# Optimization experiments

Hardware: AMD Instinct MI355X
Metric: run time of the kernel (lower is better)

The kernel has to match this reference:

```python
import jax, jax.numpy as jnp
import numpy as np

N, E, B = 10000, 20000, 500
H, NODE_D, EDGE_D, L = 64, 11, 5, 3
BN_EPS = 1e-5
STEPS = 3  # Set2Set processing steps


def setup_inputs() -> dict:
    key = jax.random.key(0)
    ks = jax.random.split(key, 16)
    s = lambda k, shape, fan: (jax.random.normal(k, shape, jnp.float32) / np.sqrt(fan)).astype(jnp.float32)
    p = {}
    p["x"] = jax.random.normal(ks[0], (N, NODE_D), jnp.float32)
    p["edge_index"] = jax.random.randint(ks[1], (2, E), 0, N)
    p["edge_attr"] = jax.random.uniform(ks[2], (E, EDGE_D), dtype=jnp.float32)
    p["batch"] = jnp.sort(jax.random.randint(ks[3], (N,), 0, B))
    # node encoder
    p["W_enc"] = s(ks[4], (NODE_D, H), NODE_D); p["b_enc"] = jnp.zeros((H,), jnp.float32)
    # per-layer NNConv block params (stacked over L layers)
    p["eW1"] = s(ks[5], (L, EDGE_D, H), EDGE_D); p["eb1"] = jnp.zeros((L, H), jnp.float32)
    p["eW2"] = s(ks[6], (L, H, H * H), H);       p["eb2"] = jnp.zeros((L, H * H), jnp.float32)
    p["root"] = s(ks[7], (L, H, H), H);          p["cbias"] = jnp.zeros((L, H), jnp.float32)
    p["gamma"] = jnp.ones((L, H), jnp.float32);  p["beta"] = jnp.zeros((L, H), jnp.float32)
    # Set2Set LSTM (input 2H, hidden H)
    p["Wih"] = s(ks[8], (4 * H, 2 * H), 2 * H); p["Whh"] = s(ks[9], (4 * H, H), H)
    p["bih"] = jnp.zeros((4 * H,), jnp.float32); p["bhh"] = jnp.zeros((4 * H,), jnp.float32)
    p["hW1"] = s(ks[10], (2 * H, H), 2 * H);   p["hb1"] = jnp.zeros((H,), jnp.float32)
    p["hW2"] = s(ks[11], (H, H // 2), H);      p["hb2"] = jnp.zeros((H // 2,), jnp.float32)
    p["hW3"] = s(ks[12], (H // 2, 1), H // 2); p["hb3"] = jnp.zeros((1,), jnp.float32)
    return p


def _forward(x, edge_attr, W_enc, b_enc, eW1, eb1, eW2, eb2, root, cbias, gamma, beta,
             Wih, Whh, bih, bhh, hW1, hb1, hW2, hb2, hW3, hb3, edge_index, batch):
    src, dst = edge_index[0], edge_index[1]
    # in-degree for mean aggregation (0-degree nodes -> 0 output, clamp avoids /0)
    deg = jax.ops.segment_sum(jnp.ones((E,), jnp.float32), dst, num_segments=N)
    deg = jnp.maximum(deg, 1.0)[:, None]

    h = jax.nn.relu(x @ W_enc + b_enc)  # [N, H]

    for l in range(L):
        residual = h
        # edge MLP -> per-edge [H, H] weight matrix
        e1 = jax.nn.relu(edge_attr @ eW1[l] + eb1[l])          # [E, H]
        W = (e1 @ eW2[l] + eb2[l]).reshape(E, H, H)            # [E, H, H]
        msg = jnp.einsum('eh,eho->eo', h[src], W)              # per-edge matvec
        agg = jax.ops.segment_sum(msg, dst, num_segments=N) / deg
        h = agg + h @ root[l] + cbias[l]                       # NNConv (root + bias)
        # BatchNorm1d (training-mode batch stats, biased var), eval-mode dropout (no-op)
        mu = jnp.mean(h, axis=0)
        var = jnp.mean((h - mu) ** 2, axis=0)
        h = (h - mu) * jax.lax.rsqrt(var + BN_EPS) * gamma[l] + beta[l]
        h = jax.nn.relu(h) + residual

    # Set2Set readout
    q_star = jnp.zeros((B, 2 * H), jnp.float32)
    hl = jnp.zeros((B, H), jnp.float32)
    cl = jnp.zeros((B, H), jnp.float32)
    for _ in range(STEPS):
        gates = q_star @ Wih.T + bih + hl @ Whh.T + bhh
        i, f, g, o = jnp.split(gates, 4, axis=1)
        cl = jax.nn.sigmoid(f) * cl + jax.nn.sigmoid(i) * jnp.tanh(g)
        hl = jax.nn.sigmoid(o) * jnp.tanh(cl)
        q = hl                                                  # [B, H]
        e = jnp.sum(h * q[batch], axis=-1)                      # [N]
        m = jax.ops.segment_max(e, batch, num_segments=B)
        ex = jnp.exp(e - m[batch])
        sden = jax.ops.segment_sum(ex, batch, num_segments=B)
        a = ex / sden[batch]                                    # per-graph softmax
        r = jax.ops.segment_sum(a[:, None] * h, batch, num_segments=B)
        q_star = jnp.concatenate([q, r], axis=1)

    # head
    z = jax.nn.relu(q_star @ hW1 + hb1)
    z = jax.nn.relu(z @ hW2 + hb2)
    out = z @ hW3 + hb3
    return out.reshape(-1)  # [B]


def reference(x, edge_index, edge_attr, batch, W_enc, b_enc, eW1, eb1, eW2, eb2, root,
              cbias, gamma, beta, Wih, Whh, bih, bhh, hW1, hb1, hW2, hb2, hW3, hb3):
    return _forward(x, edge_attr, W_enc, b_enc, eW1, eb1, eW2, eb2, root, cbias, gamma,
                    beta, Wih, Whh, bih, bhh, hW1, hb1, hW2, hb2, hW3, hb3,
                    edge_index, batch)
```

## Files before the change

kernel.cpp:

```cpp
#include <hip/hip_runtime.h>
#include <math.h>

#define ND 11
#define ED 5
#define NL 3
#define NSTEPS 3
#define BN_EPS 1e-5f
#define NSLAB 32
#define CAP 256

typedef _Float16 half8 __attribute__((ext_vector_type(8)));
typedef float f32x4 __attribute__((ext_vector_type(4)));

__device__ __forceinline__ float sigm(float x) { return 1.0f / (1.0f + expf(-x)); }

__global__ __launch_bounds__(256) void k_setup(
    const float* __restrict__ x, const float* __restrict__ Wenc,
    const float* __restrict__ benc, float* __restrict__ h0,
    _Float16* __restrict__ hh, int N,
    const int* __restrict__ dst, float* __restrict__ deg, int E,
    const int* __restrict__ batch, int* __restrict__ ptr, int B,
    const float* __restrict__ Wih, const float* __restrict__ Whh,
    const float* __restrict__ bih, const float* __restrict__ bhh,
    float* __restrict__ WihT, float* __restrict__ WhhT, float* __restrict__ gbias,
    const float* __restrict__ w2, const float* __restrict__ b2,
    _Float16* __restrict__ w2P, float* __restrict__ zp, long NZ,
    int nbEnc, int nbDeg, int nbPtr, int nbPackW, int nbPack3) {
  int bid = blockIdx.x;
  const int tid = threadIdx.x;
  if (bid < nbEnc) {
    int idx = bid * 256 + tid;
    if (idx < N * 64) {
      int n = idx >> 6, j = idx & 63;
      float acc = benc[j];
#pragma unroll
      for (int i = 0; i < ND; ++i) acc = fmaf(x[n * ND + i], Wenc[i * 64 + j], acc);
      float v = fmaxf(acc, 0.0f);
      h0[idx] = v;
      hh[idx] = (_Float16)v;
    }
    return;
  }
  bid -= nbEnc;
  if (bid < nbDeg) {
    int e = bid * 256 + tid;
    if (e < E) atomicAdd(&deg[dst[e]], 1.0f);
    return;
  }
  bid -= nbDeg;
  if (bid < nbPtr) {
    int n = bid * 256 + tid;
    if (n < N) {
      int b = batch[n];
      int pb = (n == 0) ? -1 : batch[n - 1];
      for (int g = pb + 1; g <= b; ++g) ptr[g] = n;
      if (n == N - 1)
        for (int g = b + 1; g <= B; ++g) ptr[g] = N;
    }
    return;
  }
  bid -= nbPtr;
  if (bid < nbPackW) {
    int idx = bid * 256 + tid;
    if (idx < 128 * 256) {
      int i = idx >> 8, g = idx & 255;
      WihT[i * 256 + g] = Wih[g * 128 + i];
    } else if (idx < 192 * 256) {
      int j = idx - 128 * 256;
      int i = j >> 8, g = j & 255;
      WhhT[i * 256 + g] = Whh[g * 64 + i];
    } else if (idx < 192 * 256 + 256) {
      int g = idx - 192 * 256;
      gbias[g] = bih[g] + bhh[g];
    }
    return;
  }
  bid -= nbPackW;
  if (bid < nbPack3) {
    int lay = bid / 130;
    int idx = (bid % 130) * 256 + tid;
    int l = idx & 63;
    int f = (idx >> 6) & 7;
    int s = idx >> 9;
    int nf = f >> 1, kf = f & 1;
    const float* srow = (s < 64) ? (w2 + (size_t)lay * 64 * 4096 + (size_t)s * 4096)
                                 : (b2 + (size_t)lay * 4096);
    int o = nf * 16 + (l & 15);
    int hb = kf * 32 + (l >> 4) * 8;
    half8 v;
#pragma unroll
    for (int j = 0; j < 8; ++j) v[j] = (_Float16)srow[(hb + j) * 64 + o];
    *(half8*)(w2P + ((size_t)lay * 65 * 8 * 64 + idx) * 8) = v;
    return;
  }
  bid -= nbPack3;
  {
    long i4 = ((long)bid * 256 + tid) * 4;
    if (i4 + 3 < NZ) *(float4*)(zp + i4) = make_float4(0.f, 0.f, 0.f, 0.f);
    else for (; i4 < NZ; ++i4) zp[i4] = 0.f;
  }
}

__global__ void k_zdeg(float* __restrict__ deg, int N) {
  int i = blockIdx.x * blockDim.x + threadIdx.x;
  if (i < N) deg[i] = 0.f;
}

__global__ __launch_bounds__(256) void k_scan(const float* __restrict__ deg,
                                              int* __restrict__ dptr,
                                              int* __restrict__ cursor, int N) {
  __shared__ int wsum[4];
  __shared__ int s_carry;
  const int tid = threadIdx.x, lane = tid & 63, w = tid >> 6;
  if (tid == 0) s_carry = 0;
  __syncthreads();
  for (int base = 0; base < N; base += 1024) {
    int n0 = base + tid * 4;
    int v[4];
    int s = 0;
#pragma unroll
    for (int i = 0; i < 4; ++i) { v[i] = (n0 + i < N) ? (int)deg[n0 + i] : 0; s += v[i]; }
    int sc = s;
#pragma unroll
    for (int off = 1; off < 64; off <<= 1) {
      int t = __shfl_up(sc, off);
      if (lane >= off) sc += t;
    }
    if (lane == 63) wsum[w] = sc;
    __syncthreads();
    int wpre = 0;
    for (int ww = 0; ww < w; ++ww) wpre += wsum[ww];
    int excl = s_carry + wpre + sc - s;
#pragma unroll
    for (int i = 0; i < 4; ++i) {
      if (n0 + i < N) { dptr[n0 + i] = excl; cursor[n0 + i] = excl; }
      excl += v[i];
    }
    __syncthreads();
    if (tid == 255) s_carry += wsum[0] + wsum[1] + wsum[2] + wsum[3];
    __syncthreads();
  }
  if (threadIdx.x == 0) dptr[N] = s_carry;
}

__global__ void k_fill(const int* __restrict__ dst, const int* __restrict__ src,
                       int* __restrict__ cursor, int* __restrict__ perm,
                       int* __restrict__ srcP, int* __restrict__ dstP, int E) {
  int e = blockIdx.x * blockDim.x + threadIdx.x;
  if (e < E) {
    int d = dst[e];
    int slot = atomicAdd(&cursor[d], 1);
    perm[slot] = e;
    srcP[slot] = src[e];
    dstP[slot] = d;
  }
}

__global__ __launch_bounds__(256) void k_hmat(
    const float* __restrict__ hn, const float* __restrict__ hp,
    const float* __restrict__ slab, const float* __restrict__ gm,
    const float* __restrict__ bt, float* __restrict__ hout,
    _Float16* __restrict__ hh, int N) {
  __shared__ float stats[128];
  const int tid = threadIdx.x;
  if (tid < 128) {
    float s = 0.f;
#pragma unroll
    for (int sl = 0; sl < NSLAB; ++sl) s += slab[sl * 128 + tid];
    stats[tid] = s;
  }
  __syncthreads();
  int idx = blockIdx.x * 256 + tid;
  if (idx >= N * 64) return;
  int o = idx & 63;
  float invN = 1.0f / (float)N;
  float mu = stats[o] * invN;
  float var = stats[64 + o] * invN - mu * mu;
  float rs = rsqrtf(var + BN_EPS) * gm[o];
  float v = fmaxf((hn[idx] - mu) * rs + bt[o], 0.f) + hp[idx];
  hout[idx] = v;
  hh[idx] = (_Float16)v;
}

__global__ __launch_bounds__(512, 4) void k_msgagg(
    const float* __restrict__ ea, const int* __restrict__ perm,
    const float* __restrict__ eW1l, const float* __restrict__ eb1l,
    const _Float16* __restrict__ hh, const int* __restrict__ srcP,
    const int* __restrict__ dstP, const int* __restrict__ dptr,
    const _Float16* __restrict__ w2P, float* __restrict__ agg, int E, int N) {
  __shared__ _Float16 e1t[65][64];
  __shared__ float tileH[2][64][66];
  __shared__ float eat[64][ED];
  __shared__ float w1s[ED * 64];
  __shared__ float b1s[64];

  const int tid = threadIdx.x;
  const int wid = tid >> 6, l = tid & 63;
  const int half = wid >> 2, quad = wid & 3;
  const int lo = l & 15, lg = l >> 4;
  const int e0 = blockIdx.x * 64;

  half8 hsf[4][2];
#pragma unroll
  for (int m = 0; m < 4; ++m) {
    int s = e0 + m * 16 + lo;
    if (s < E) {
      const _Float16* hr = hh + (size_t)srcP[s] * 64;
      hsf[m][0] = *(const half8*)(hr + lg * 8);
      hsf[m][1] = *(const half8*)(hr + 32 + lg * 8);
    } else {
      half8 z = {0, 0, 0, 0, 0, 0, 0, 0};
      hsf[m][0] = z;
      hsf[m][1] = z;
    }
  }

  if (tid < ED * 64) w1s[tid] = eW1l[tid];
  else if (tid < ED * 64 + 64) b1s[tid - ED * 64] = eb1l[tid - ED * 64];
  if (tid >= 448) {
    int s = e0 + (tid - 448);
    if (s < E) {
      int e = perm[s];
#pragma unroll
      for (int i = 0; i < ED; ++i) eat[tid - 448][i] = ea[(size_t)e * ED + i];
    } else {
#pragma unroll
      for (int i = 0; i < ED; ++i) eat[tid - 448][i] = 0.f;
    }
  }
  __syncthreads();

  for (int idx = tid; idx < 65 * 64; idx += 512) {
    int el = idx & 63, k = idx >> 6;
    float v = 1.0f;
    if (k < 64) {
      v = b1s[k];
#pragma unroll
      for (int i = 0; i < ED; ++i) v = fmaf(eat[el][i], w1s[i * 64 + k], v);
      v = fmaxf(v, 0.f);
    }
    e1t[k][el] = (_Float16)v;
  }
  __syncthreads();

  const int kb = half ? 32 : 0;
  f32x4 acc[4] = {};
  const half8* wp = (const half8*)w2P;
  half8 Br[2][2];
#pragma unroll
  for (int d = 0; d < 2; ++d) {
    Br[d][0] = wp[((size_t)(kb + d) * 8 + quad * 2 + 0) * 64 + l];
    Br[d][1] = wp[((size_t)(kb + d) * 8 + quad * 2 + 1) * 64 + l];
  }
#pragma unroll 33
  for (int i = 0; i < 33; ++i) {
    const int d = i & 1;
    const int k = kb + i;
    const bool zslice = (half && i == 0);
#pragma unroll
    for (int m = 0; m < 4; ++m) {
      const _Float16 s16 = zslice ? (_Float16)0.f : e1t[k][m * 16 + lo];
      half8 A0 = hsf[m][0] * s16;
      half8 A1 = hsf[m][1] * s16;
      acc[m] = __builtin_amdgcn_mfma_f32_16x16x32_f16(A0, Br[d][0], acc[m], 0, 0, 0);
      acc[m] = __builtin_amdgcn_mfma_f32_16x16x32_f16(A1, Br[d][1], acc[m], 0, 0, 0);
    }
    if (i + 2 < 33) {
      Br[d][0] = wp[((size_t)(kb + i + 2) * 8 + quad * 2 + 0) * 64 + l];
      Br[d][1] = wp[((size_t)(kb + i + 2) * 8 + quad * 2 + 1) * 64 + l];
    }
  }

#pragma unroll
  for (int m = 0; m < 4; ++m)
#pragma unroll
    for (int r = 0; r < 4; ++r)
      tileH[half][m * 16 + lg * 4 + r][quad * 16 + lo] = acc[m][r];
  __syncthreads();

  const int o = tid & 63, r8 = tid >> 6;
  const int lastSlot = (e0 + 63 < E) ? (e0 + 63) : (E - 1);
  int nLo = dstP[e0], nHi = dstP[lastSlot];
  nLo = (nLo < 0) ? 0 : ((nLo >= N) ? N - 1 : nLo);
  nHi = (nHi < 0) ? 0 : ((nHi >= N) ? N - 1 : nHi);
  for (int nn = nLo + r8; nn <= nHi; nn += 8) {
    int d0 = dptr[nn], d1 = dptr[nn + 1];
    d0 = (d0 < 0) ? 0 : d0;
    d1 = (d1 > E) ? E : d1;
    int j0 = (d0 > e0) ? d0 : e0;
    int j1 = (d1 < e0 + 64) ? d1 : (e0 + 64);
    float sum = 0.f;
    for (int j = j0; j < j1; ++j) sum += tileH[0][j - e0][o] + tileH[1][j - e0][o];
    float* dp = agg + (size_t)nn * 64 + o;
    if (d0 < e0 || d1 > e0 + 64) { if (j1 > j0) atomicAdd(dp, sum); }
    else *dp = sum;
  }
}

__global__ __launch_bounds__(256) void k_update(
    const float* __restrict__ hcur, float* __restrict__ agg,
    const float* __restrict__ deg, const float* __restrict__ root,
    const float* __restrict__ cb, float* __restrict__ hn_out,
    float* __restrict__ slab_out, int N) {
  __shared__ float hrow[16][64];
  __shared__ float red[2][256];
  const int tid = threadIdx.x, o = tid & 63, r = tid >> 6;
  const int nb = blockIdx.x * 16;
#pragma unroll
  for (int ii = 0; ii < 4; ++ii) {
    int n = nb + ii * 4 + r;
    hrow[ii * 4 + r][o] = (n < N) ? hcur[(size_t)n * 64 + o] : 0.f;
  }
  __syncthreads();
  float acc[4] = {0.f, 0.f, 0.f, 0.f};
  for (int c = 0; c < 64; ++c) {
    float rv = root[c * 64 + o];
#pragma unroll
    for (int ii = 0; ii < 4; ++ii) acc[ii] = fmaf(hrow[ii * 4 + r][c], rv, acc[ii]);
  }
  float s = 0.f, ss = 0.f;
  const float cbv = cb[o];
#pragma unroll
  for (int ii = 0; ii < 4; ++ii) {
    int n = nb + ii * 4 + r;
    if (n < N) {
      float a = agg[(size_t)n * 64 + o];
      agg[(size_t)n * 64 + o] = 0.f;
      float v = acc[ii] + cbv + a / fmaxf(deg[n], 1.0f);
      hn_out[(size_t)n * 64 + o] = v;
      s += v;
      ss += v * v;
    }
  }
  red[0][tid] = s;
  red[1][tid] = ss;
  __syncthreads();
  if (r == 0) {
    float t0 = red[0][o] + red[0][64 + o] + red[0][128 + o] + red[0][192 + o];
    float t1 = red[1][o] + red[1][64 + o] + red[1][128 + o] + red[1][192 + o];
    float* sl = slab_out + (size_t)(blockIdx.x & (NSLAB - 1)) * 128;
    atomicAdd(&sl[o], t0);
    atomicAdd(&sl[64 + o], t1);
  }
}

__global__ __launch_bounds__(256) void k_s2s_all(
    const float* __restrict__ hn2, const float* __restrict__ h2,
    const float* __restrict__ slab2, const float* __restrict__ gm,
    const float* __restrict__ bt, const int* __restrict__ ptr,
    const float* __restrict__ WihT, const float* __restrict__ WhhT,
    const float* __restrict__ gbias,
    const float* __restrict__ hW1, const float* __restrict__ hb1,
    const float* __restrict__ hW2, const float* __restrict__ hb2,
    const float* __restrict__ hW3, const float* __restrict__ hb3,
    float* __restrict__ out, int N) {
  __shared__ float hvs[CAP * 65];
  __shared__ float stats[128];
  __shared__ float mu_s[64], rs_s[64], bt_s[64];
  __shared__ float qs[128];
  __shared__ float hlc[64], clc[64];
  __shared__ float gates[256];
  __shared__ float qv[64];
  __shared__ float ev[256];
  __shared__ float av[CAP];
  __shared__ float redM[4], redS[4];
  __shared__ float redR[4][64];
  __shared__ float z1[64], z2[32];
  const int b = blockIdx.x, tid = threadIdx.x;
  const int wid = tid >> 6, lane = tid & 63;

  if (tid < 128) {
    float s = 0.f;
#pragma unroll
    for (int sl = 0; sl < NSLAB; ++sl) s += slab2[sl * 128 + tid];
    stats[tid] = s;
    qs[tid] = 0.f;
  }
  if (tid < 64) { hlc[tid] = 0.f; clc[tid] = 0.f; }
  __syncthreads();
  if (tid < 64) {
    float invN = 1.0f / (float)N;
    float mu = stats[tid] * invN;
    float var = stats[64 + tid] * invN - mu * mu;
    mu_s[tid] = mu;
    rs_s[tid] = rsqrtf(var + BN_EPS) * gm[tid];
    bt_s[tid] = bt[tid];
  }
  __syncthreads();
  int beg = ptr[b], end = ptr[b + 1];
  if (beg < 0) beg = 0;
  if (end > N) end = N;
  const int nn = (end > beg) ? (end - beg) : 0;
  const bool big = nn > CAP;

  if (!big) {
    for (int idx = tid; idx < nn * 64; idx += 256) {
      int n = idx >> 6, o = idx & 63;
      size_t g = (size_t)(beg + n) * 64 + o;
      hvs[n * 65 + o] = fmaxf((hn2[g] - mu_s[o]) * rs_s[o] + bt_s[o], 0.f) + h2[g];
    }
  }
  __syncthreads();

  for (int step = 0; step < NSTEPS; ++step) {
    float g = gbias[tid];
    for (int i = 0; i < 128; ++i) g = fmaf(qs[i], WihT[i * 256 + tid], g);
    for (int i = 0; i < 64; ++i) g = fmaf(hlc[i], WhhT[i * 256 + tid], g);
    gates[tid] = g;
    __syncthreads();
    if (tid < 64) {
      float ig = sigm(gates[tid]);
      float fg = sigm(gates[64 + tid]);
      float gg = tanhf(gates[128 + tid]);
      float og = sigm(gates[192 + tid]);
      float c = fg * clc[tid] + ig * gg;
      clc[tid] = c;
      float hnew = og * tanhf(c);
      hlc[tid] = hnew;
      qv[tid] = hnew;
    }
    __syncthreads();

    if (!big) {
      if (tid < nn) {
        float s = 0.f;
#pragma unroll 8
        for (int o = 0; o < 64; ++o) s = fmaf(hvs[tid * 65 + o], qv[o], s);
        ev[tid] = s;
      } else {
        ev[tid] = -INFINITY;
      }
      __syncthreads();
      if (tid < 64) {
        float m4 = fmaxf(fmaxf(ev[tid], ev[64 + tid]), fmaxf(ev[128 + tid], ev[192 + tid]));
#pragma unroll
        for (int s = 32; s; s >>= 1) m4 = fmaxf(m4, __shfl_xor(m4, s));
        if (tid == 0) redM[0] = m4;
      }
      __syncthreads();
      const float m = redM[0];
      float a = 0.f;
      if (tid < nn) { a = expf(ev[tid] - m); av[tid] = a; }
      __syncthreads();
      ev[tid] = a;
      __syncthreads();
      if (tid < 64) {
        float s4 = ev[tid] + ev[64 + tid] + ev[128 + tid] + ev[192 + tid];
#pragma unroll
        for (int s = 32; s; s >>= 1) s4 += __shfl_xor(s4, s);
        if (tid == 0) redS[0] = s4;
      }
      __syncthreads();
      const float sden = redS[0];
      if (tid < 128) {
        if (tid < 64) {
          qs[tid] = qv[tid];
        } else {
          int o = tid - 64;
          float r = 0.f;
          for (int n = 0; n < nn; ++n) r = fmaf(av[n], hvs[n * 65 + o], r);
          qs[tid] = (nn > 0) ? r / sden : 0.f;
        }
      }
      __syncthreads();
    } else {
      const float q = qv[lane];
      float mw = -INFINITY;
      for (int n = beg + wid; n < end; n += 4) {
        float hv = fmaxf((hn2[(size_t)n * 64 + lane] - mu_s[lane]) * rs_s[lane] + bt_s[lane],
                         0.f) + h2[(size_t)n * 64 + lane];
        float p = hv * q;
#pragma unroll
        for (int s = 32; s; s >>= 1) p += __shfl_xor(p, s);
        mw = fmaxf(mw, p);
      }
      if (lane == 0) redM[wid] = mw;
      __syncthreads();
      const float m = fmaxf(fmaxf(redM[0], redM[1]), fmaxf(redM[2], redM[3]));
      float ssum = 0.f, racc = 0.f;
      for (int n = beg + wid; n < end; n += 4) {
        float hv = fmaxf((hn2[(size_t)n * 64 + lane] - mu_s[lane]) * rs_s[lane] + bt_s[lane],
                         0.f) + h2[(size_t)n * 64 + lane];
        float p = hv * q;
#pragma unroll
        for (int s = 32; s; s >>= 1) p += __shfl_xor(p, s);
        float a = expf(p - m);
        ssum += a;
        racc = fmaf(a, hv, racc);
      }
      if (lane == 0) redS[wid] = ssum;
      redR[wid][lane] = racc;
      __syncthreads();
      if (tid < 128) {
        if (tid < 64) {
          qs[tid] = qv[tid];
        } else {
          int o2 = tid - 64;
          float rsum = redR[0][o2] + redR[1][o2] + redR[2][o2] + redR[3][o2];
          float sd = redS[0] + redS[1] + redS[2] + redS[3];
          qs[tid] = (end > beg) ? rsum / sd : 0.0f;
        }
      }
      __syncthreads();
    }
  }

  if (tid < 64) {
    float a = hb1[tid];
    for (int i = 0; i < 128; ++i) a = fmaf(qs[i], hW1[i * 64 + tid], a);
    z1[tid] = fmaxf(a, 0.0f);
  }
  __syncthreads();
  if (tid < 32) {
    float a2 = hb2[tid];
    for (int i = 0; i < 64; ++i) a2 = fmaf(z1[i], hW2[i * 32 + tid], a2);
    z2[tid] = fmaxf(a2, 0.0f);
  }
  __syncthreads();
  if (tid < 64) {
    float p = (tid < 32) ? z2[tid] * hW3[tid] : 0.0f;
#pragma unroll
    for (int s = 32; s; s >>= 1) p += __shfl_xor(p, s);
    if (tid == 0) out[b] = p + hb3[0];
  }
}

extern "C" void kernel_launch(void* const* d_in, const int* in_sizes, int n_in,
                              void* d_out, int out_size, void* d_ws, size_t ws_size,
                              hipStream_t stream) {
  const float* x = (const float*)d_in[0];
  const int* eidx = (const int*)d_in[1];
  const float* ea = (const float*)d_in[2];
  const int* batch = (const int*)d_in[3];
  const float* Wenc = (const float*)d_in[4];
  const float* benc = (const float*)d_in[5];
  const float* eW1 = (const float*)d_in[6];
  const float* eb1 = (const float*)d_in[7];
  const float* eW2 = (const float*)d_in[8];
  const float* eb2 = (const float*)d_in[9];
  const float* root = (const float*)d_in[10];
  const float* cbias = (const float*)d_in[11];
  const float* gamma = (const float*)d_in[12];
  const float* beta = (const float*)d_in[13];
  const float* Wih = (const float*)d_in[14];
  const float* Whh = (const float*)d_in[15];
  const float* bih = (const float*)d_in[16];
  const float* bhh = (const float*)d_in[17];
  const float* hW1 = (const float*)d_in[18];
  const float* hb1 = (const float*)d_in[19];
  const float* hW2 = (const float*)d_in[20];
  const float* hb2 = (const float*)d_in[21];
  const float* hW3 = (const float*)d_in[22];
  const float* hb3 = (const float*)d_in[23];

  const int N = in_sizes[0] / ND;
  const int E = in_sizes[1] / 2;
  const int B = out_size;
  const int* srcp = eidx;
  const int* dstp = eidx + E;
  const int Etiles = (E + 63) / 64;

  float* ws = (float*)d_ws;
  float* deg = ws;
  float* agg = deg + N;
  float* bnslab = agg + (size_t)N * 64;
  const long NZ = (long)((size_t)N * 64 + NL * NSLAB * 128);
  float* h0 = bnslab + NL * NSLAB * 128;
  float* h1 = h0 + (size_t)N * 64;
  float* h2 = h1 + (size_t)N * 64;
  float* hn0 = h2 + (size_t)N * 64;
  float* hn1 = hn0 + (size_t)N * 64;
  float* hn2 = hn1 + (size_t)N * 64;
  _Float16* w2P = (_Float16*)(hn2 + (size_t)N * 64);
  _Float16* hhalf = w2P + (size_t)3 * 65 * 8 * 64 * 8;
  float* WihT = (float*)(hhalf + (size_t)N * 64);
  float* WhhT = WihT + 128 * 256;
  float* gbias = WhhT + 64 * 256;
  int* dptr = (int*)(gbias + 256);
  int* cursor = dptr + N + 1;
  int* perm = cursor + N;
  int* srcP = perm + E;
  int* dstP = srcP + E;
  int* ptr = dstP + E;

  const int nbEnc = (N * 64 + 255) / 256;
  const int nbDeg = (E + 255) / 256;
  const int nbPtr = (N + 255) / 256;
  const int nbPackW = (192 * 256 + 256 + 255) / 256;
  const int nbPack3 = 130 * NL;
  const int nbZero = (int)((NZ / 4 + 255) / 256);

  k_zdeg<<<(N + 255) / 256, 256, 0, stream>>>(deg, N);
  k_setup<<<nbEnc + nbDeg + nbPtr + nbPackW + nbPack3 + nbZero, 256, 0, stream>>>(
      x, Wenc, benc, h0, hhalf, N, dstp, deg, E, batch, ptr, B,
      Wih, Whh, bih, bhh, WihT, WhhT, gbias, eW2, eb2, w2P, agg, NZ,
      nbEnc, nbDeg, nbPtr, nbPackW, nbPack3);
  k_scan<<<1, 256, 0, stream>>>(deg, dptr, cursor, N);
  k_fill<<<(E + 255) / 256, 256, 0, stream>>>(dstp, srcp, cursor, perm, srcP, dstP, E);

  float* hbuf[3] = {h0, h1, h2};
  float* hnbuf[3] = {hn0, hn1, hn2};
  for (int l = 0; l < NL; ++l) {
    float* slab_l = bnslab + (size_t)l * NSLAB * 128;
    const _Float16* w2_l = w2P + (size_t)l * 65 * 8 * 64 * 8;
    if (l > 0) {
      k_hmat<<<(N * 64 + 255) / 256, 256, 0, stream>>>(
          hnbuf[l - 1], hbuf[l - 1], bnslab + (size_t)(l - 1) * NSLAB * 128,
          gamma + (l - 1) * 64, beta + (l - 1) * 64, hbuf[l], hhalf, N);
    }
    k_msgagg<<<Etiles, 512, 0, stream>>>(ea, perm, eW1 + (size_t)l * ED * 64,
                                         eb1 + (size_t)l * 64, hhalf, srcP, dstP, dptr,
                                         w2_l, agg, E, N);
    k_update<<<(N + 15) / 16, 256, 0, stream>>>(hbuf[l], agg, deg,
                                                root + (size_t)l * 64 * 64,
                                                cbias + l * 64, hnbuf[l], slab_l, N);
  }

  k_s2s_all<<<B, 256, 0, stream>>>(hn2, h2, bnslab + (size_t)2 * NSLAB * 128,
                                   gamma + 2 * 64, beta + 2 * 64, ptr, WihT, WhhT, gbias,
                                   hW1, hb1, hW2, hb2, hW3, hb3, (float*)d_out, N);
}
```

Measured before the change: 181.7 us.

## Process two graphs per Set2Set block with one wavefront per graph

The Set2Set kernel now handles two graphs per block. The LSTM gate matvec is shared across both graphs, so each weight load from WihT/WhhT is reused twice. Attention, softmax and readout run per graph inside a single wavefront using shuffles, which removes most of the block-wide barriers. Shared staging is cut from 256 to 64 nodes per graph, so graphs with more than 64 nodes fall back to a slower global-memory path that walks nodes serially in one wave. Half as many blocks are launched.

New measurement: 184.6 us. Within noise of the previous version (+1.6%).

```diff
diff --git a/kernel.cpp b/kernel.cpp
--- a/kernel.cpp
+++ b/kernel.cpp
@@ -7,7 +7,8 @@
 #define NSTEPS 3
 #define BN_EPS 1e-5f
 #define NSLAB 32
-#define CAP 256
+#define NG 2
+#define SCAP 64
 
 typedef _Float16 half8 __attribute__((ext_vector_type(8)));
 typedef float f32x4 __attribute__((ext_vector_type(4)));
@@ -353,30 +354,43 @@
     const float* __restrict__ hW1, const float* __restrict__ hb1,
     const float* __restrict__ hW2, const float* __restrict__ hb2,
     const float* __restrict__ hW3, const float* __restrict__ hb3,
-    float* __restrict__ out, int N) {
-  __shared__ float hvs[CAP * 65];
+    float* __restrict__ out, int N, int B) {
+  __shared__ float hvs[NG][SCAP][65];
   __shared__ float stats[128];
   __shared__ float mu_s[64], rs_s[64], bt_s[64];
-  __shared__ float qs[128];
-  __shared__ float hlc[64], clc[64];
-  __shared__ float gates[256];
-  __shared__ float qv[64];
-  __shared__ float ev[256];
-  __shared__ float av[CAP];
-  __shared__ float redM[4], redS[4];
-  __shared__ float redR[4][64];
-  __shared__ float z1[64], z2[32];
-  const int b = blockIdx.x, tid = threadIdx.x;
+  __shared__ float qs[NG][128];
+  __shared__ float hlc[NG][64], clc[NG][64];
+  __shared__ float gates[NG][256];
+  __shared__ float qv[NG][64];
+  __shared__ float av[NG][64];
+  __shared__ int gbeg[NG], gend[NG], gnn[NG];
+  __shared__ float z1s[NG][64], z2s[NG][32];
+  const int tid = threadIdx.x;
   const int wid = tid >> 6, lane = tid & 63;
+  const int g0 = blockIdx.x * NG;
 
   if (tid < 128) {
     float s = 0.f;
 #pragma unroll
     for (int sl = 0; sl < NSLAB; ++sl) s += slab2[sl * 128 + tid];
     stats[tid] = s;
-    qs[tid] = 0.f;
-  }
-  if (tid < 64) { hlc[tid] = 0.f; clc[tid] = 0.f; }
+    hlc[tid >> 6][tid & 63] = 0.f;
+    clc[tid >> 6][tid & 63] = 0.f;
+  }
+  {
+    qs[tid >> 7][tid & 127] = 0.f;
+  }
+  if (tid < NG) {
+    int gb = g0 + tid;
+    int bg = 0, en = 0;
+    if (gb < B) {
+      bg = ptr[gb]; en = ptr[gb + 1];
+      if (bg < 0) bg = 0;
+      if (en > N) en = N;
+      if (en < bg) en = bg;
+    }
+    gbeg[tid] = bg; gend[tid] = en; gnn[tid] = en - bg;
+  }
   __syncthreads();
   if (tid < 64) {
     float invN = 1.0f / (float)N;
@@ -387,141 +401,114 @@
     bt_s[tid] = bt[tid];
   }
   __syncthreads();
-  int beg = ptr[b], end = ptr[b + 1];
-  if (beg < 0) beg = 0;
-  if (end > N) end = N;
-  const int nn = (end > beg) ? (end - beg) : 0;
-  const bool big = nn > CAP;
-
-  if (!big) {
-    for (int idx = tid; idx < nn * 64; idx += 256) {
-      int n = idx >> 6, o = idx & 63;
-      size_t g = (size_t)(beg + n) * 64 + o;
-      hvs[n * 65 + o] = fmaxf((hn2[g] - mu_s[o]) * rs_s[o] + bt_s[o], 0.f) + h2[g];
+
+#pragma unroll
+  for (int gg = 0; gg < NG; ++gg) {
+    int nn = gnn[gg], bg = gbeg[gg];
+    if (nn <= SCAP) {
+      for (int idx = tid; idx < nn * 64; idx += 256) {
+        int n = idx >> 6, o = idx & 63;
+        size_t g = (size_t)(bg + n) * 64 + o;
+        hvs[gg][n][o] = fmaxf((hn2[g] - mu_s[o]) * rs_s[o] + bt_s[o], 0.f) + h2[g];
+      }
     }
   }
   __syncthreads();
 
   for (int step = 0; step < NSTEPS; ++step) {
-    float g = gbias[tid];
-    for (int i = 0; i < 128; ++i) g = fmaf(qs[i], WihT[i * 256 + tid], g);
-    for (int i = 0; i < 64; ++i) g = fmaf(hlc[i], WhhT[i * 256 + tid], g);
-    gates[tid] = g;
+    float a0 = gbias[tid], a1 = gbias[tid];
+    for (int i = 0; i < 128; ++i) {
+      float wv = WihT[i * 256 + tid];
+      a0 = fmaf(qs[0][i], wv, a0);
+      a1 = fmaf(qs[1][i], wv, a1);
+    }
+    for (int i = 0; i < 64; ++i) {
+      float wv = WhhT[i * 256 + tid];
+      a0 = fmaf(hlc[0][i], wv, a0);
+      a1 = fmaf(hlc[1][i], wv, a1);
+    }
+    gates[0][tid] = a0;
+    gates[1][tid] = a1;
     __syncthreads();
-    if (tid < 64) {
-      float ig = sigm(gates[tid]);
-      float fg = sigm(gates[64 + tid]);
-      float gg = tanhf(gates[128 + tid]);
-      float og = sigm(gates[192 + tid]);
-      float c = fg * clc[tid] + ig * gg;
-      clc[tid] = c;
+    if (tid < 128) {
+      int g = tid >> 6, j = tid & 63;
+      float ig = sigm(gates[g][j]);
+      float fg = sigm(gates[g][64 + j]);
+      float gg = tanhf(gates[g][128 + j]);
+      float og = sigm(gates[g][192 + j]);
+      float c = fg * clc[g][j] + ig * gg;
+      clc[g][j] = c;
       float hnew = og * tanhf(c);
-      hlc[tid] = hnew;
-      qv[tid] = hnew;
+      hlc[g][j] = hnew;
+      qv[g][j] = hnew;
     }
     __syncthreads();
-
-    if (!big) {
-      if (tid < nn) {
-        float s = 0.f;
+    if (wid < NG && g0 + wid < B) {
+      const int g = wid;
+      const int nn = gnn[g], bg = gbeg[g], en = gend[g];
+      if (nn <= SCAP) {
+        float e = -INFINITY;
+        if (lane < nn) {
+          float s = 0.f;
 #pragma unroll 8
-        for (int o = 0; o < 64; ++o) s = fmaf(hvs[tid * 65 + o], qv[o], s);
-        ev[tid] = s;
+          for (int o = 0; o < 64; ++o) s = fmaf(hvs[g][lane][o], qv[g][o], s);
+          e = s;
+        }
+        float m = e;
+#pragma unroll
+        for (int s = 32; s; s >>= 1) m = fmaxf(m, __shfl_xor(m, s));
+        float a = (lane < nn) ? expf(e - m) : 0.f;
+        av[g][lane] = a;
+        float ssum = a;
+#pragma unroll
+        for (int s = 32; s; s >>= 1) ssum += __shfl_xor(ssum, s);
+        float r = 0.f;
+        for (int n = 0; n < nn; ++n) r = fmaf(av[g][n], hvs[g][n][lane], r);
+        qs[g][lane] = qv[g][lane];
+        qs[g][64 + lane] = (nn > 0) ? r / ssum : 0.f;
       } else {
-        ev[tid] = -INFINITY;
+        const float q = qv[g][lane];
+        float m = -INFINITY;
+        for (int n = bg; n < en; ++n) {
+          float hv = fmaxf((hn2[(size_t)n * 64 + lane] - mu_s[lane]) * rs_s[lane] +
+                               bt_s[lane], 0.f) + h2[(size_t)n * 64 + lane];
+          float p = hv * q;
+#pragma unroll
+          for (int s = 32; s; s >>= 1) p += __shfl_xor(p, s);
+          m = fmaxf(m, p);
+        }
+        float ssum = 0.f, racc = 0.f;
+        for (int n = bg; n < en; ++n) {
+          float hv = fmaxf((hn2[(size_t)n * 64 + lane] - mu_s[lane]) * rs_s[lane] +
+                               bt_s[lane], 0.f) + h2[(size_t)n * 64 + lane];
+          float p = hv * q;
+#pragma unroll
+          for (int s = 32; s; s >>= 1) p += __shfl_xor(p, s);
+          float a = expf(p - m);
+          ssum += a;
+          racc = fmaf(a, hv, racc);
+        }
+        qs[g][lane] = q;
+        qs[g][64 + lane] = (en > bg) ? racc / ssum : 0.f;
       }
-      __syncthreads();
-      if (tid < 64) {
-        float m4 = fmaxf(fmaxf(ev[tid], ev[64 + tid]), fmaxf(ev[128 + tid], ev[192 + tid]));
-#pragma unroll
-        for (int s = 32; s; s >>= 1) m4 = fmaxf(m4, __shfl_xor(m4, s));
-        if (tid == 0) redM[0] = m4;
-      }
-      __syncthreads();
-      const float m = redM[0];
-      float a = 0.f;
-      if (tid < nn) { a = expf(ev[tid] - m); av[tid] = a; }
-      __syncthreads();
-      ev[tid] = a;
-      __syncthreads();
-      if (tid < 64) {
-        float s4 = ev[tid] + ev[64 + tid] + ev[128 + tid] + ev[192 + tid];
-#pragma unroll
-        for (int s = 32; s; s >>= 1) s4 += __shfl_xor(s4, s);
-        if (tid == 0) redS[0] = s4;
-      }
-      __syncthreads();
-      const float sden = redS[0];
-      if (tid < 128) {
-        if (tid < 64) {
-          qs[tid] = qv[tid];
-        } else {
-          int o = tid - 64;
-          float r = 0.f;
-          for (int n = 0; n < nn; ++n) r = fmaf(av[n], hvs[n * 65 + o], r);
-          qs[tid] = (nn > 0) ? r / sden : 0.f;
-        }
-      }
-      __syncthreads();
-    } else {
-      const float q = qv[lane];
-      float mw = -INFINITY;
-      for (int n = beg + wid; n < end; n += 4) {
-        float hv = fmaxf((hn2[(size_t)n * 64 + lane] - mu_s[lane]) * rs_s[lane] + bt_s[lane],
-                         0.f) + h2[(size_t)n * 64 + lane];
-        float p = hv * q;
-#pragma unroll
-        for (int s = 32; s; s >>= 1) p += __shfl_xor(p, s);
-        mw = fmaxf(mw, p);
-      }
-      if (lane == 0) redM[wid] = mw;
-      __syncthreads();
-      const float m = fmaxf(fmaxf(redM[0], redM[1]), fmaxf(redM[2], redM[3]));
-      float ssum = 0.f, racc = 0.f;
-      for (int n = beg + wid; n < end; n += 4) {
-        float hv = fmaxf((hn2[(size_t)n * 64 + lane] - mu_s[lane]) * rs_s[lane] + bt_s[lane],
-                         0.f) + h2[(size_t)n * 64 + lane];
-        float p = hv * q;
-#pragma unroll
-        for (int s = 32; s; s >>= 1) p += __shfl_xor(p, s);
-        float a = expf(p - m);
-        ssum += a;
-        racc = fmaf(a, hv, racc);
-      }
-      if (lane == 0) redS[wid] = ssum;
-      redR[wid][lane] = racc;
-      __syncthreads();
-      if (tid < 128) {
-        if (tid < 64) {
-          qs[tid] = qv[tid];
-        } else {
-          int o2 = tid - 64;
-          float rsum = redR[0][o2] + redR[1][o2] + redR[2][o2] + redR[3][o2];
-          float sd = redS[0] + redS[1] + redS[2] + redS[3];
-          qs[tid] = (end > beg) ? rsum / sd : 0.0f;
-        }
-      }
-      __syncthreads();
-    }
-  }
-
-  if (tid < 64) {
-    float a = hb1[tid];
-    for (int i = 0; i < 128; ++i) a = fmaf(qs[i], hW1[i * 64 + tid], a);
-    z1[tid] = fmaxf(a, 0.0f);
-  }
-  __syncthreads();
-  if (tid < 32) {
-    float a2 = hb2[tid];
-    for (int i = 0; i < 64; ++i) a2 = fmaf(z1[i], hW2[i * 32 + tid], a2);
-    z2[tid] = fmaxf(a2, 0.0f);
-  }
-  __syncthreads();
-  if (tid < 64) {
-    float p = (tid < 32) ? z2[tid] * hW3[tid] : 0.0f;
+    }
+    __syncthreads();
+  }
+
+  if (wid < NG && g0 + wid < B) {
+    const int g = wid;
+    float a = hb1[lane];
+    for (int i = 0; i < 128; ++i) a = fmaf(qs[g][i], hW1[i * 64 + lane], a);
+    z1s[g][lane] = fmaxf(a, 0.0f);
+    if (lane < 32) {
+      float a2 = hb2[lane];
+      for (int i = 0; i < 64; ++i) a2 = fmaf(z1s[g][i], hW2[i * 32 + lane], a2);
+      z2s[g][lane] = fmaxf(a2, 0.0f);
+    }
+    float p = (lane < 32) ? z2s[g][lane] * hW3[lane] : 0.0f;
 #pragma unroll
     for (int s = 32; s; s >>= 1) p += __shfl_xor(p, s);
-    if (tid == 0) out[b] = p + hb3[0];
+    if (lane == 0) out[g0 + g] = p + hb3[0];
   }
 }
 
@@ -616,7 +603,7 @@
                                                 cbias + l * 64, hnbuf[l], slab_l, N);
   }
 
-  k_s2s_all<<<B, 256, 0, stream>>>(hn2, h2, bnslab + (size_t)2 * NSLAB * 128,
-                                   gamma + 2 * 64, beta + 2 * 64, ptr, WihT, WhhT, gbias,
-                                   hW1, hb1, hW2, hb2, hW3, hb3, (float*)d_out, N);
-}
+  k_s2s_all<<<(B + NG - 1) / NG, 256, 0, stream>>>(
+      hn2, h2, bnslab + (size_t)2 * NSLAB * 128, gamma + 2 * 64, beta + 2 * 64, ptr,
+      WihT, WhhT, gbias, hW1, hb1, hW2, hb2, hW3, hb3, (float*)d_out, N, B);
+}
```
